# Kernel optimization log

Hardware: AMD Instinct MI355X
Metric: run time of the kernel (lower is better)

## Reference

```python
import jax, jax.numpy as jnp
import numpy as np

D_MODEL = 768
N_HEADS = 8
Q_RANK = 64
KV_RANK = 64
ROPE_DIM = 64
NOPE_DIM = D_MODEL // N_HEADS - ROPE_DIM  # 32
V_DIM = D_MODEL // N_HEADS               # 96
Q_HEAD_DIM = NOPE_DIM + ROPE_DIM         # 96
EPS = 1e-6
ROPE_BASE = 10000.0


def rms_norm(x, w, eps=EPS):
    v = jnp.mean(jnp.square(x.astype(jnp.float32)), axis=-1, keepdims=True)
    return (x.astype(jnp.float32) * jax.lax.rsqrt(v + eps)).astype(x.dtype) * w


def rope_cos_sin(seq_len, dim):
    inv_freq = 1.0 / (ROPE_BASE ** (jnp.arange(0, dim, 2, dtype=jnp.float32) / dim))
    freqs = jnp.outer(jnp.arange(seq_len, dtype=jnp.float32), inv_freq)
    emb = jnp.concatenate([freqs, freqs], axis=-1)  # [s, dim]
    return jnp.cos(emb), jnp.sin(emb)


def apply_rope(x, cos, sin, pos_ids):
    # x: [b,h,s,d]; DeepSeek-V2 de-interleaves pairs before rotate_half
    b, h, s, d = x.shape
    x = x.reshape(b, h, s, d // 2, 2).transpose(0, 1, 2, 4, 3).reshape(b, h, s, d)
    c = cos[pos_ids][:, None]  # [b,1,s,d]
    sn = sin[pos_ids][:, None]
    x1, x2 = jnp.split(x, 2, axis=-1)
    rot = jnp.concatenate([-x2, x1], axis=-1)
    return x * c + rot * sn


def setup_inputs() -> dict:
    key = jax.random.key(0)
    ks = jax.random.split(key, 8)
    s = 0.02
    return {
        "src": jax.random.normal(ks[0], (4, 2048, D_MODEL), jnp.float32),
        "wq_a": jax.random.normal(ks[1], (Q_RANK, D_MODEL), jnp.float32) * s,
        "q_a_ln_w": jnp.ones((Q_RANK,), jnp.float32),
        "wq_b": jax.random.normal(ks[2], (N_HEADS * Q_HEAD_DIM, Q_RANK), jnp.float32) * s,
        "wkv_a": jax.random.normal(ks[3], (KV_RANK + ROPE_DIM, D_MODEL), jnp.float32) * s,
        "kv_a_ln_w": jnp.ones((KV_RANK,), jnp.float32),
        "wkv_b": jax.random.normal(ks[4], (N_HEADS * (NOPE_DIM + V_DIM), KV_RANK), jnp.float32) * s,
        "wo": jax.random.normal(ks[5], (D_MODEL, N_HEADS * V_DIM), jnp.float32) * s,
        "norm_w": jnp.ones((D_MODEL,), jnp.float32),
    }


def reference(src, wq_a, q_a_ln_w, wq_b, wkv_a, kv_a_ln_w, wkv_b, wo, norm_w):
    b, s, _ = src.shape
    pos = jnp.broadcast_to(jnp.arange(s)[None], (b, s))
    cos, sin = rope_cos_sin(s, ROPE_DIM)

    # ---- compress_kv (torch.no_grad in original) ----
    ckv = src @ wkv_a.T                                  # [b,s,rank+rope]
    c_lat, k_pe = ckv[..., :KV_RANK], ckv[..., KV_RANK:]
    c_lat = rms_norm(c_lat, kv_a_ln_w)
    k_pe = apply_rope(k_pe[:, None], cos, sin, pos)[:, 0]  # [b,s,rope]
    c_lat = jax.lax.stop_gradient(c_lat)
    k_pe = jax.lax.stop_gradient(k_pe)

    # ---- query path ----
    q = rms_norm(src @ wq_a.T, q_a_ln_w) @ wq_b.T        # [b,s,h*96]
    q = q.reshape(b, s, N_HEADS, Q_HEAD_DIM).transpose(0, 2, 1, 3)
    q_nope, q_pe = q[..., :NOPE_DIM], q[..., NOPE_DIM:]
    q_pe = apply_rope(q_pe, cos, sin, pos)

    # ---- absorb kv_b_proj ----
    w = wkv_b.reshape(N_HEADS, NOPE_DIM + V_DIM, KV_RANK)
    q_absorb, out_absorb = w[:, :NOPE_DIM], w[:, NOPE_DIM:]   # [h,32,r], [h,96,r]
    q_lat = jnp.einsum('bhsd,hdr->bhsr', q_nope, q_absorb)    # [b,h,s,r]

    scale = Q_HEAD_DIM ** -0.5
    scores = (jnp.einsum('bhsr,btr->bhst', q_lat, c_lat)
              + jnp.einsum('bhsd,btd->bhst', q_pe, k_pe)) * scale
    attn = jax.nn.softmax(scores.astype(jnp.float32), axis=-1).astype(src.dtype)

    ctx = jnp.einsum('bhst,btr->bhsr', attn, c_lat)           # [b,h,s,r]
    ctx = jnp.einsum('bhsr,hvr->bhsv', ctx, out_absorb)       # [b,h,s,96]
    attn_out = ctx.transpose(0, 2, 1, 3).reshape(b, s, N_HEADS * V_DIM) @ wo.T

    # residual (dropout in eval = identity) + RMSNorm
    return rms_norm(src + attn_out, norm_w)
```

## Files before the change

### kernel.cpp

```cpp
#include <hip/hip_runtime.h>


#define DEV static __device__ __forceinline__
typedef unsigned short ushort_t;
typedef __attribute__((ext_vector_type(8))) short bf8_t;
typedef __attribute__((ext_vector_type(4))) float f4_t;

DEV float bf2f(unsigned int u) {
    union { float f; unsigned int i; } x; x.i = u << 16; return x.f;
}
DEV ushort_t f2bf(float f) {
    union { float f; unsigned int u; } x; x.f = f;
    unsigned int u = x.u;
    return (ushort_t)((u + 0x7fffu + ((u >> 16) & 1u)) >> 16);
}
DEV float ldin(const void* p, size_t i, int isbf) {
    return isbf ? bf2f(((const ushort_t*)p)[i]) : ((const float*)p)[i];
}
DEV float fexp2(float x) {
#if __has_builtin(__builtin_amdgcn_exp2f)
    return __builtin_amdgcn_exp2f(x);
#else
    return exp2f(x);
#endif
}
DEV int get_isbf(const void* nw) {
    return ((((const unsigned int*)nw)[0] & 0xffffu) != 0u) ? 1 : 0;
}

constexpr int   TOK   = 4 * 2048;
constexpr float EPSF  = 1e-6f;
constexpr float QSCALE = (float)(0.10206207261596575 * 1.4426950408889634);
constexpr float L2_10000_OVER_32 = 0.4152410118609203f;

constexpr size_t OFF_WOT   = 0;
constexpr size_t OFF_WKVAT = 589824;
constexpr size_t OFF_WQAT  = 688128;
constexpr size_t OFF_WQBT  = 737280;
constexpr size_t OFF_QAF   = 786432;
constexpr size_t OFF_OAT   = 802816;
constexpr size_t OFF_QLN   = 851968;
constexpr size_t OFF_KVLN  = 852032;
constexpr size_t OFF_NW    = 852096;
constexpr size_t OFF_FLAG  = 852864;
constexpr size_t OFF_CTXF  = 852880;
constexpr size_t OFF_SRCBF = 3998608;
constexpr size_t OFF_KBF   = 7144336;
constexpr size_t OFF_VTB   = 7668624;
constexpr size_t OFF_QBF   = 7930768;
constexpr size_t OFF_ROPE  = 12125072;

constexpr int PB0 = 2304;
constexpr int PB1 = PB0 + 384;
constexpr int PB2 = PB1 + 192;
constexpr int PB3 = PB2 + 192;
constexpr int PB4 = PB3 + 64;
constexpr int PB5 = PB4 + 192;
constexpr int PB6 = PB5 + 4;
constexpr int PB7 = PB6 + 256;

__global__ __launch_bounds__(256) void prep_k(
    const void* __restrict__ wq_a, const void* __restrict__ q_ln,
    const void* __restrict__ wq_b, const void* __restrict__ wkv_a,
    const void* __restrict__ kv_ln, const void* __restrict__ wkv_b,
    const void* __restrict__ wo, const void* __restrict__ nw,
    float* __restrict__ ws)
{
    const int isbf = get_isbf(nw);
    const int bid = blockIdx.x;
    const int tid = threadIdx.x;
    if (bid < PB0) {
        int i = bid * 256 + tid;
        ushort_t* wob = (ushort_t*)(ws + OFF_WOT);
        wob[i] = isbf ? ((const ushort_t*)wo)[i] : f2bf(((const float*)wo)[i]);
    } else if (bid < PB1) {
        int i = (bid - PB0) * 256 + tid;
        ushort_t* d = (ushort_t*)(ws + OFF_WKVAT);
        d[i] = isbf ? ((const ushort_t*)wkv_a)[i] : f2bf(((const float*)wkv_a)[i]);
    } else if (bid < PB2) {
        int i = (bid - PB1) * 256 + tid;
        ushort_t* d = (ushort_t*)(ws + OFF_WQAT);
        d[i] = isbf ? ((const ushort_t*)wq_a)[i] : f2bf(((const float*)wq_a)[i]);
    } else if (bid < PB3) {
        int i = (bid - PB2) * 256 + tid;
        ushort_t* d = (ushort_t*)(ws + OFF_WQBT);
        d[i] = isbf ? ((const ushort_t*)wq_b)[i] : f2bf(((const float*)wq_b)[i]);
    } else if (bid < PB4) {
        int i = (bid - PB3) * 256 + tid;
        int h = i >> 11, rem = i & 2047, r = rem >> 5, d = rem & 31;
        ushort_t* dst = (ushort_t*)(ws + OFF_QAF);
        dst[i] = f2bf(ldin(wkv_b, (size_t)(h * 128 + d) * 64 + r, isbf) * QSCALE);
    } else if (bid < PB5) {
        int i = (bid - PB4) * 256 + tid;
        int h = i / 6144, rem = i - h * 6144;
        int r = rem / 96, v = rem - r * 96;
        ws[OFF_OAT + i] = ldin(wkv_b, (size_t)h * 8192 + 2048 + v * 64 + r, isbf);
    } else if (bid < PB6) {
        int i = (bid - PB5) * 256 + tid;
        if (i < 64)             ws[OFF_QLN + i]       = ldin(q_ln, i, isbf);
        else if (i < 128)       ws[OFF_KVLN + i - 64] = ldin(kv_ln, i - 64, isbf);
        else if (i < 128 + 768) ws[OFF_NW + i - 128]  = ldin(nw, i - 128, isbf);
    } else {
        int i = (bid - PB6) * 256 + tid;
        int pos = i >> 5, p = i & 31;
        float inv = exp2f(-(float)p * L2_10000_OVER_32);
        float ang = (float)pos * inv;
        float2* tab = (float2*)(ws + OFF_ROPE);
        tab[i] = make_float2(cosf(ang), sinf(ang));
    }
}

__global__ __launch_bounds__(512) void k1_ckv(
    const void* __restrict__ src, const void* __restrict__ nw,
    const float* __restrict__ ws,
    ushort_t* __restrict__ Kbf, ushort_t* __restrict__ VTbf,
    ushort_t* __restrict__ srcbf)
{
    const ushort_t* wkvab = (const ushort_t*)(ws + OFF_WKVAT);
    const float* kvln  = ws + OFF_KVLN;
    const float2* tab  = (const float2*)(ws + OFF_ROPE);
    const int isbf = get_isbf(nw);
    __shared__ __align__(16) ushort_t sA[32 * 776];
    __shared__ float ckv[32][132];
    int j = threadIdx.x;
    int t0 = blockIdx.x * 32;
    int w = j >> 6, lane = j & 63;
    int tl = lane & 15, qd = lane >> 4;

    {
        for (int e = j; e < 32 * 96; e += 512) {
            int row = e / 96, c8 = e - row * 96;
            size_t off = (size_t)(t0 + row) * 768 + c8 * 8;
            if (isbf) {
                uint4 v = *(const uint4*)((const ushort_t*)src + off);
                *(uint4*)(sA + row * 776 + c8 * 8) = v;
            } else {
                const float4* p = (const float4*)((const float*)src + off);
                float4 f0 = p[0], f1 = p[1];
                ushort_t tmp[8] = {f2bf(f0.x), f2bf(f0.y), f2bf(f0.z), f2bf(f0.w),
                                   f2bf(f1.x), f2bf(f1.y), f2bf(f1.z), f2bf(f1.w)};
                uint4 v = *(const uint4*)tmp;
                *(uint4*)(sA + row * 776 + c8 * 8) = v;
                *(uint4*)(srcbf + off) = v;
            }
        }
    }
    __syncthreads();
    {
        f4_t acc[2];
        acc[0] = (f4_t){0.f, 0.f, 0.f, 0.f};
        acc[1] = (f4_t){0.f, 0.f, 0.f, 0.f};
        const ushort_t* bp = wkvab + (size_t)(w * 16 + tl) * 768 + qd * 8;
#pragma unroll 4
        for (int ks = 0; ks < 24; ++ks) {
            bf8_t b  = *(const bf8_t*)(bp + ks * 32);
            bf8_t a0 = *(const bf8_t*)(sA + tl * 776 + ks * 32 + qd * 8);
            bf8_t a1 = *(const bf8_t*)(sA + (16 + tl) * 776 + ks * 32 + qd * 8);
            acc[0] = __builtin_amdgcn_mfma_f32_16x16x32_bf16(a0, b, acc[0], 0, 0, 0);
            acc[1] = __builtin_amdgcn_mfma_f32_16x16x32_bf16(a1, b, acc[1], 0, 0, 0);
        }
#pragma unroll
        for (int mt = 0; mt < 2; ++mt)
#pragma unroll
            for (int r = 0; r < 4; ++r)
                ckv[mt * 16 + qd * 4 + r][w * 16 + tl] = acc[mt][r];
    }
    __syncthreads();

    if (j < 256) {
        int tt = j >> 3, l = j & 7;
        float ss = 0.f;
#pragma unroll
        for (int i = 0; i < 8; ++i) { float v = ckv[tt][l * 8 + i]; ss += v * v; }
        ss += __shfl_xor(ss, 1); ss += __shfl_xor(ss, 2); ss += __shfl_xor(ss, 4);
        float rs = rsqrtf(ss * (1.f / 64.f) + EPSF);
        size_t base = (size_t)(t0 + tt) * 128;
        ushort_t kb[8];
        float clw[8];
#pragma unroll
        for (int i = 0; i < 8; ++i) {
            int o2 = l * 8 + i;
            float cl = ckv[tt][o2] * rs;
            if (isbf) cl = bf2f(f2bf(cl));
            clw[i] = cl * kvln[o2];
            kb[i] = f2bf(clw[i]);
        }
        uint4 pack;
        pack.x = kb[0] | ((unsigned)kb[1] << 16); pack.y = kb[2] | ((unsigned)kb[3] << 16);
        pack.z = kb[4] | ((unsigned)kb[5] << 16); pack.w = kb[6] | ((unsigned)kb[7] << 16);
        *(uint4*)&Kbf[base + l * 8] = pack;
        int pos = (t0 + tt) & 2047;
        ushort_t r0[4], r1[4];
#pragma unroll
        for (int i = 0; i < 4; ++i) {
            int p = l * 4 + i;
            float2 cssn = tab[pos * 32 + p];
            float e = ckv[tt][64 + 2 * p], od = ckv[tt][64 + 2 * p + 1];
            r0[i] = f2bf(e * cssn.x - od * cssn.y);
            r1[i] = f2bf(od * cssn.x + e * cssn.y);
        }
        uint2 p0, p1;
        p0.x = r0[0] | ((unsigned)r0[1] << 16); p0.y = r0[2] | ((unsigned)r0[3] << 16);
        p1.x = r1[0] | ((unsigned)r1[1] << 16); p1.y = r1[2] | ((unsigned)r1[3] << 16);
        *(uint2*)&Kbf[base + 64 + l * 4] = p0;
        *(uint2*)&Kbf[base + 96 + l * 4] = p1;
#pragma unroll
        for (int i = 0; i < 8; ++i) ckv[tt][l * 8 + i] = clw[i];
    }
    __syncthreads();
    if (j < 256) {
        int t = j & 31, rb = (j >> 5) * 8;
        int bb = t0 >> 11, col = (t0 & 2047) + t;
#pragma unroll
        for (int i = 0; i < 8; ++i) {
            int r = rb + i;
            VTbf[((size_t)(bb * 64 + r)) * 2048 + col] = f2bf(ckv[t][r]);
        }
    }
}

__global__ __launch_bounds__(128) void k2a_qn(
    const void* __restrict__ src, const void* __restrict__ nw,
    const float* __restrict__ ws, ushort_t* __restrict__ qn_all)
{
    const int isbf = get_isbf(nw);
    const ushort_t* srcb = isbf ? (const ushort_t*)src : (const ushort_t*)(ws + OFF_SRCBF);
    const ushort_t* wqab = (const ushort_t*)(ws + OFF_WQAT);
    const float*    qln  = ws + OFF_QLN;
    __shared__ __align__(16) ushort_t LDS[2 * 1152];
    int j = threadIdx.x;
    int w = j >> 6, lane = j & 63;
    int tl = lane & 15, qd = lane >> 4;
    ushort_t* tmpn = LDS + w * 1152;
    int tokw = blockIdx.x * 16;

    f4_t C1[4];
#pragma unroll
    for (int nt = 0; nt < 4; ++nt) C1[nt] = (f4_t){0.f, 0.f, 0.f, 0.f};
    {
        const ushort_t* ap = srcb + (size_t)(tokw + tl) * 768 + qd * 8;
#pragma unroll 4
        for (int ks = 0; ks < 24; ++ks) {
            bf8_t a = *(const bf8_t*)(ap + ks * 32);
#pragma unroll
            for (int nt = 0; nt < 4; ++nt) {
                bf8_t bfr = *(const bf8_t*)(wqab + (size_t)(nt * 16 + tl) * 768 + ks * 32 + qd * 8);
                C1[nt] = __builtin_amdgcn_mfma_f32_16x16x32_bf16(a, bfr, C1[nt], 0, 0, 0);
            }
        }
    }
    float rsv[4];
#pragma unroll
    for (int r = 0; r < 4; ++r) {
        float s = C1[0][r] * C1[0][r] + C1[1][r] * C1[1][r]
                + C1[2][r] * C1[2][r] + C1[3][r] * C1[3][r];
        s += __shfl_xor(s, 1); s += __shfl_xor(s, 2);
        s += __shfl_xor(s, 4); s += __shfl_xor(s, 8);
        rsv[r] = rsqrtf(s * (1.f / 64.f) + EPSF);
    }
    float qlnv[4];
#pragma unroll
    for (int nt = 0; nt < 4; ++nt) qlnv[nt] = qln[nt * 16 + tl];
#pragma unroll
    for (int nt = 0; nt < 4; ++nt)
#pragma unroll
        for (int r = 0; r < 4; ++r) {
            float v = C1[nt][r] * rsv[r];
            if (isbf) v = bf2f(f2bf(v));
            tmpn[(qd * 4 + r) * 72 + nt * 16 + tl] = f2bf(v * qlnv[nt]);
        }
    if (w == 0) {
#pragma unroll
        for (int i = 0; i < 2; ++i) {
            int e = i * 64 + lane;
            int row = e >> 3, ch = e & 7;
            uint4 v = *(const uint4*)(tmpn + row * 72 + ch * 8);
            *(uint4*)(qn_all + (size_t)(tokw + row) * 64 + ch * 8) = v;
        }
    }
}

__global__ __launch_bounds__(512) void k2b_q(
    const float* __restrict__ ws, const ushort_t* __restrict__ qn_all,
    ushort_t* __restrict__ Qbf)
{
    const ushort_t* wqbb = (const ushort_t*)(ws + OFF_WQBT);
    const ushort_t* qabs = (const ushort_t*)(ws + OFF_QAF);
    const float2*   tab  = (const float2*)(ws + OFF_ROPE);

    __shared__ __align__(16) ushort_t sB[384 * 72];
    __shared__ __align__(16) ushort_t sA[32 * 72];
    __shared__ __align__(16) ushort_t PW[8 * 2816];
    int j = threadIdx.x;
    int bx = blockIdx.x;
    int t0 = (bx >> 1) * 32;
    int colh = (bx & 1) * 384;
    int w = j >> 6, lane = j & 63;
    int tl = lane & 15, qd = lane >> 4;
    int mt = w & 1, hh = w >> 1;
    int h = (bx & 1) * 4 + hh;
    ushort_t* qnb = PW + w * 2816;
    ushort_t* qf  = qnb + 640;
    int tokw = t0 + mt * 16;

    {
        for (int e = j; e < 384 * 8; e += 512) {
            int rr = e >> 3, ch = e & 7;
            uint4 v = *(const uint4*)(wqbb + (size_t)(colh + rr) * 64 + ch * 8);
            *(uint4*)(sB + rr * 72 + ch * 8) = v;
        }
    }
    if (j < 256) {
        int rr = j >> 3, ch = j & 7;
        uint4 v = *(const uint4*)(qn_all + (size_t)(t0 + rr) * 64 + ch * 8);
        *(uint4*)(sA + rr * 72 + ch * 8) = v;
    }
    __syncthreads();

    bf8_t A2[2];
#pragma unroll
    for (int ks = 0; ks < 2; ++ks)
        A2[ks] = *(const bf8_t*)(sA + (mt * 16 + tl) * 72 + ks * 32 + qd * 8);

    float csv[4][4], snv[4][4];
#pragma unroll
    for (int nt2 = 0; nt2 < 4; ++nt2) {
        int p = (nt2 * 16 + tl) >> 1;
#pragma unroll
        for (int r = 0; r < 4; ++r) {
            int pos = (tokw + qd * 4 + r) & 2047;
            float2 t = tab[pos * 32 + p];
            csv[nt2][r] = t.x * QSCALE;
            snv[nt2][r] = t.y * QSCALE;
        }
    }
    const bool evn = !(tl & 1);
    int bb = tokw >> 11, pos0 = tokw & 2047;

    f4_t C2[6];
#pragma unroll
    for (int nt = 0; nt < 6; ++nt) C2[nt] = (f4_t){0.f, 0.f, 0.f, 0.f};
#pragma unroll
    for (int nt = 0; nt < 6; ++nt)
#pragma unroll
        for (int ks = 0; ks < 2; ++ks) {
            bf8_t bfr = *(const bf8_t*)(sB + (hh * 96 + nt * 16 + tl) * 72 + ks * 32 + qd * 8);
            C2[nt] = __builtin_amdgcn_mfma_f32_16x16x32_bf16(A2[ks], bfr, C2[nt], 0, 0, 0);
        }
#pragma unroll
    for (int nt = 0; nt < 2; ++nt)
#pragma unroll
        for (int r = 0; r < 4; ++r)
            qnb[(qd * 4 + r) * 40 + nt * 16 + tl] = f2bf(C2[nt][r]);
    bf8_t an = *(const bf8_t*)(qnb + tl * 40 + qd * 8);
    f4_t C3[4];
#pragma unroll
    for (int nt = 0; nt < 4; ++nt) C3[nt] = (f4_t){0.f, 0.f, 0.f, 0.f};
#pragma unroll
    for (int nt = 0; nt < 4; ++nt) {
        bf8_t bfr = *(const bf8_t*)(qabs + (size_t)h * 2048 + (nt * 16 + tl) * 32 + qd * 8);
        C3[nt] = __builtin_amdgcn_mfma_f32_16x16x32_bf16(an, bfr, C3[nt], 0, 0, 0);
    }
#pragma unroll
    for (int nt = 0; nt < 4; ++nt)
#pragma unroll
        for (int r = 0; r < 4; ++r)
            qf[(qd * 4 + r) * 136 + nt * 16 + tl] = f2bf(C3[nt][r]);
#pragma unroll
    for (int nt2 = 0; nt2 < 4; ++nt2) {
        int p = (nt2 * 16 + tl) >> 1;
        int outc = evn ? (64 + p) : (96 + p);
#pragma unroll
        for (int r = 0; r < 4; ++r) {
            float val = C2[nt2 + 2][r];
            float part = __shfl_xor(val, 1);
            float res = evn ? (val * csv[nt2][r] - part * snv[nt2][r])
                            : (val * csv[nt2][r] + part * snv[nt2][r]);
            qf[(qd * 4 + r) * 136 + outc] = f2bf(res);
        }
    }
    size_t qb = ((size_t)(bb * 8 + h) * 2048 + pos0) * 128;
#pragma unroll
    for (int i = 0; i < 4; ++i) {
        int idx = i * 64 + lane;
        int row = idx >> 4, c = idx & 15;
        uint4 v = *(const uint4*)(qf + row * 136 + c * 8);
        *(uint4*)(Qbf + qb + (size_t)row * 128 + c * 8) = v;
    }
}

__global__ __launch_bounds__(256, 2) void k3_attn(
    const ushort_t* __restrict__ Qbf, const ushort_t* __restrict__ Kbf,
    const ushort_t* __restrict__ VTbf, const float* __restrict__ oaT,
    ushort_t* __restrict__ ctxb)
{
    __shared__ __align__(16) ushort_t LDS[22528];
    ushort_t* Kt = LDS;
    ushort_t* Vt = LDS + 8704;
    ushort_t* Pw = LDS + 13312;
    int j = threadIdx.x;
    int b = blockIdx.z, h = blockIdx.y, q0g = blockIdx.x * 128;
    int w = j >> 6, lane = j & 63;
    int tl = lane & 15, qd = lane >> 4;
    ushort_t* Pme = Pw + w * 2304;
    int qw = q0g + w * 32;

    bf8_t qfA[4], qfB[4];
    {
        const ushort_t* qp = Qbf + ((size_t)((b * 8 + h) * 2048) + qw + tl) * 128 + qd * 8;
#pragma unroll
        for (int ks = 0; ks < 4; ++ks) {
            qfA[ks] = *(const bf8_t*)(qp + ks * 32);
            qfB[ks] = *(const bf8_t*)(qp + 16 * 128 + ks * 32);
        }
    }
    f4_t OaccA[4], OaccB[4];
#pragma unroll
    for (int nt = 0; nt < 4; ++nt) {
        OaccA[nt] = (f4_t){0.f, 0.f, 0.f, 0.f};
        OaccB[nt] = (f4_t){0.f, 0.f, 0.f, 0.f};
    }
    float lA = 0.f, lB = 0.f;

    const size_t kbase = (size_t)b * 2048 * 128;
    const size_t vbase = (size_t)b * 64 * 2048;

    for (int it = 0; it < 32; ++it) {
        __syncthreads();
        {
            int r = j >> 2, c0 = (j & 3) * 32;
            const uint4* gp = (const uint4*)(Kbf + kbase + (size_t)(it * 64 + r) * 128 + c0);
            uint4 a0 = gp[0], a1 = gp[1], a2 = gp[2], a3 = gp[3];
            uint4* dp = (uint4*)(Kt + r * 136 + c0);
            dp[0] = a0; dp[1] = a1; dp[2] = a2; dp[3] = a3;
        }
        {
            int d = j >> 2, c0 = (j & 3) * 16;
            const uint4* gp = (const uint4*)(VTbf + vbase + (size_t)d * 2048 + it * 64 + c0);
            uint4 a0 = gp[0], a1 = gp[1];
            uint4* dp = (uint4*)(Vt + d * 72 + c0);
            dp[0] = a0; dp[1] = a1;
        }
        __syncthreads();
        f4_t SA[4], SB[4];
        __builtin_amdgcn_s_setprio(1);
#pragma unroll
        for (int nt = 0; nt < 4; ++nt) {
            f4_t cA = (f4_t){0.f, 0.f, 0.f, 0.f};
            f4_t cB = (f4_t){0.f, 0.f, 0.f, 0.f};
#pragma unroll
            for (int ks = 0; ks < 4; ++ks) {
                bf8_t kf = *(const bf8_t*)(Kt + (nt * 16 + tl) * 136 + ks * 32 + qd * 8);
                cA = __builtin_amdgcn_mfma_f32_16x16x32_bf16(kf, qfA[ks], cA, 0, 0, 0);
                cB = __builtin_amdgcn_mfma_f32_16x16x32_bf16(kf, qfB[ks], cB, 0, 0, 0);
            }
            SA[nt] = cA; SB[nt] = cB;
        }
        __builtin_amdgcn_s_setprio(0);
        float rsA = 0.f, rsB = 0.f;
#pragma unroll
        for (int nt = 0; nt < 4; ++nt)
#pragma unroll
            for (int r = 0; r < 4; ++r) {
                float pA = fexp2(SA[nt][r]); SA[nt][r] = pA; rsA += pA;
                float pB = fexp2(SB[nt][r]); SB[nt][r] = pB; rsB += pB;
            }
        rsA += __shfl_xor(rsA, 16); rsA += __shfl_xor(rsA, 32);
        rsB += __shfl_xor(rsB, 16); rsB += __shfl_xor(rsB, 32);
        lA += rsA; lB += rsB;
#pragma unroll
        for (int nt = 0; nt < 4; ++nt) {
            uint2 pkA, pkB;
            pkA.x = f2bf(SA[nt][0]) | ((unsigned)f2bf(SA[nt][1]) << 16);
            pkA.y = f2bf(SA[nt][2]) | ((unsigned)f2bf(SA[nt][3]) << 16);
            pkB.x = f2bf(SB[nt][0]) | ((unsigned)f2bf(SB[nt][1]) << 16);
            pkB.y = f2bf(SB[nt][2]) | ((unsigned)f2bf(SB[nt][3]) << 16);
            *(uint2*)(Pme + tl * 72 + nt * 16 + qd * 4) = pkA;
            *(uint2*)(Pme + (16 + tl) * 72 + nt * 16 + qd * 4) = pkB;
        }
        bf8_t pfA[2], pfB[2];
#pragma unroll
        for (int ks = 0; ks < 2; ++ks) {
            pfA[ks] = *(const bf8_t*)(Pme + tl * 72 + ks * 32 + qd * 8);
            pfB[ks] = *(const bf8_t*)(Pme + (16 + tl) * 72 + ks * 32 + qd * 8);
        }
        __builtin_amdgcn_s_setprio(1);
#pragma unroll
        for (int nt = 0; nt < 4; ++nt)
#pragma unroll
            for (int ks = 0; ks < 2; ++ks) {
                bf8_t vf = *(const bf8_t*)(Vt + (nt * 16 + tl) * 72 + ks * 32 + qd * 8);
                OaccA[nt] = __builtin_amdgcn_mfma_f32_16x16x32_bf16(pfA[ks], vf, OaccA[nt], 0, 0, 0);
                OaccB[nt] = __builtin_amdgcn_mfma_f32_16x16x32_bf16(pfB[ks], vf, OaccB[nt], 0, 0, 0);
            }
        __builtin_amdgcn_s_setprio(0);
    }
    {
        float linvA[4], linvB[4];
#pragma unroll
        for (int r = 0; r < 4; ++r) {
            float lqA = __shfl(lA, (lane & 48) + qd * 4 + r);
            float lqB = __shfl(lB, (lane & 48) + qd * 4 + r);
            linvA[r] = 1.f / lqA; linvB[r] = 1.f / lqB;
        }
#pragma unroll
        for (int nt = 0; nt < 4; ++nt)
#pragma unroll
            for (int r = 0; r < 4; ++r) {
                Pme[(qd * 4 + r) * 72 + nt * 16 + tl] = f2bf(OaccA[nt][r] * linvA[r]);
                Pme[(16 + qd * 4 + r) * 72 + nt * 16 + tl] = f2bf(OaccB[nt][r] * linvB[r]);
            }
    }
    __syncthreads();
    ushort_t* OA = LDS;
    for (int e = j; e < 96 * 64; e += 256) {
        int v = e >> 6, r = e & 63;
        OA[v * 72 + r] = f2bf(oaT[h * 6144 + r * 96 + v]);
    }
    __syncthreads();
    {
        bf8_t ofA[2], ofB[2];
#pragma unroll
        for (int ks = 0; ks < 2; ++ks) {
            ofA[ks] = *(const bf8_t*)(Pme + tl * 72 + ks * 32 + qd * 8);
            ofB[ks] = *(const bf8_t*)(Pme + (16 + tl) * 72 + ks * 32 + qd * 8);
        }
        __builtin_amdgcn_s_setprio(1);
#pragma unroll
        for (int nt = 0; nt < 6; ++nt) {
            f4_t cA = (f4_t){0.f, 0.f, 0.f, 0.f};
            f4_t cB = (f4_t){0.f, 0.f, 0.f, 0.f};
#pragma unroll
            for (int ks = 0; ks < 2; ++ks) {
                bf8_t af = *(const bf8_t*)(OA + (nt * 16 + tl) * 72 + ks * 32 + qd * 8);
                cA = __builtin_amdgcn_mfma_f32_16x16x32_bf16(ofA[ks], af, cA, 0, 0, 0);
                cB = __builtin_amdgcn_mfma_f32_16x16x32_bf16(ofB[ks], af, cB, 0, 0, 0);
            }
#pragma unroll
            for (int r = 0; r < 4; ++r) {
                size_t tokA = (size_t)(b * 2048 + qw + qd * 4 + r);
                size_t tokB = tokA + 16;
                ctxb[tokA * 768 + h * 96 + nt * 16 + tl] = f2bf(cA[r]);
                ctxb[tokB * 768 + h * 96 + nt * 16 + tl] = f2bf(cB[r]);
            }
        }
        __builtin_amdgcn_s_setprio(0);
    }
}

__global__ __launch_bounds__(512, 2) void k5a_gemm(
    const void* __restrict__ src, const void* __restrict__ nw,
    const float* __restrict__ ws,
    const ushort_t* __restrict__ ctxb, ushort_t* __restrict__ ybf)
{
    const ushort_t* woB = (const ushort_t*)(ws + OFF_WOT);
    const int isbf = get_isbf(nw);
    __shared__ __align__(16) ushort_t sB[384 * 72];
    __shared__ __align__(16) ushort_t sA[32 * 72];
    int j = threadIdx.x;
    int bx = blockIdx.x;
    int t0 = (bx >> 1) * 32;
    int colh = (bx & 1) * 384;
    int w = j >> 6, lane = j & 63;
    int tl = lane & 15, qd = lane >> 4;
    int mt = w & 1;
    int n0l = (w >> 1) * 96;

    f4_t acc[6];
#pragma unroll
    for (int nt = 0; nt < 6; ++nt) acc[nt] = (f4_t){0.f, 0.f, 0.f, 0.f};

    for (int kb = 0; kb < 12; ++kb) {
        __syncthreads();
        {
            for (int e = j; e < 384 * 8; e += 512) {
                int rr = e >> 3, ch = e & 7;
                uint4 v = *(const uint4*)(woB + (size_t)(colh + rr) * 768 + kb * 64 + ch * 8);
                *(uint4*)(sB + rr * 72 + ch * 8) = v;
            }
        }
        if (j < 256) {
            int rr = j >> 3, ch = j & 7;
            uint4 v = *(const uint4*)(ctxb + (size_t)(t0 + rr) * 768 + kb * 64 + ch * 8);
            *(uint4*)(sA + rr * 72 + ch * 8) = v;
        }
        __syncthreads();
        __builtin_amdgcn_s_setprio(1);
#pragma unroll
        for (int ks = 0; ks < 2; ++ks) {
            bf8_t a = *(const bf8_t*)(sA + (mt * 16 + tl) * 72 + ks * 32 + qd * 8);
#pragma unroll
            for (int nt = 0; nt < 6; ++nt) {
                bf8_t bfr = *(const bf8_t*)(sB + (n0l + nt * 16 + tl) * 72 + ks * 32 + qd * 8);
                acc[nt] = __builtin_amdgcn_mfma_f32_16x16x32_bf16(a, bfr, acc[nt], 0, 0, 0);
            }
        }
        __builtin_amdgcn_s_setprio(0);
    }
#pragma unroll
    for (int nt = 0; nt < 6; ++nt)
#pragma unroll
        for (int r = 0; r < 4; ++r) {
            int row = t0 + mt * 16 + qd * 4 + r;
            int col = colh + n0l + nt * 16 + tl;
            float yv = acc[nt][r] + ldin(src, (size_t)row * 768 + col, isbf);
            ybf[(size_t)row * 768 + col] = f2bf(yv);
        }
}

__global__ __launch_bounds__(256) void k5b_norm(
    const void* __restrict__ nw_in, const float* __restrict__ ws,
    const ushort_t* __restrict__ ybf, void* __restrict__ out)
{
    const float* nw = ws + OFF_NW;
    const int isbf = get_isbf(nw_in);
    int j = threadIdx.x;
    int tt = j >> 4, s = j & 15;
    size_t row = (size_t)blockIdx.x * 16 + tt;
    const ushort_t* yp = ybf + row * 768 + s * 48;

    float val[48];
    float ss = 0.f;
#pragma unroll
    for (int c8 = 0; c8 < 6; ++c8) {
        union { uint4 u; ushort_t h[8]; } uu;
        uu.u = ((const uint4*)yp)[c8];
#pragma unroll
        for (int c = 0; c < 8; ++c) {
            float v = bf2f(uu.h[c]);
            val[c8 * 8 + c] = v;
            ss += v * v;
        }
    }
    ss += __shfl_xor(ss, 1); ss += __shfl_xor(ss, 2);
    ss += __shfl_xor(ss, 4); ss += __shfl_xor(ss, 8);
    float rs = rsqrtf(ss * (1.f / 768.f) + EPSF);
    const float* nwp = nw + s * 48;
    size_t base = row * 768 + s * 48;
    if (isbf) {
        ushort_t* op = (ushort_t*)out + base;
#pragma unroll
        for (int c8 = 0; c8 < 6; ++c8) {
            union { uint4 u; ushort_t h[8]; } uu;
#pragma unroll
            for (int c = 0; c < 8; ++c) {
                float hv = bf2f(f2bf(val[c8 * 8 + c] * rs));
                uu.h[c] = f2bf(hv * nwp[c8 * 8 + c]);
            }
            ((uint4*)op)[c8] = uu.u;
        }
    } else {
        float* op = (float*)out + base;
#pragma unroll
        for (int c4 = 0; c4 < 12; ++c4) {
            float4 f;
            f.x = val[c4 * 4 + 0] * rs * nwp[c4 * 4 + 0];
            f.y = val[c4 * 4 + 1] * rs * nwp[c4 * 4 + 1];
            f.z = val[c4 * 4 + 2] * rs * nwp[c4 * 4 + 2];
            f.w = val[c4 * 4 + 3] * rs * nwp[c4 * 4 + 3];
            ((float4*)op)[c4] = f;
        }
    }
}

extern "C" void kernel_launch(void* const* d_in, const int* in_sizes, int n_in,
                              void* d_out, int out_size, void* d_ws, size_t ws_size,
                              hipStream_t stream)
{
    const void* src   = d_in[0];
    const void* wq_a  = d_in[1];
    const void* q_ln  = d_in[2];
    const void* wq_b  = d_in[3];
    const void* wkv_a = d_in[4];
    const void* kv_ln = d_in[5];
    const void* wkv_b = d_in[6];
    const void* wo    = d_in[7];
    const void* nw    = d_in[8];
    float* ws = (float*)d_ws;
    ushort_t* Kbf   = (ushort_t*)(ws + OFF_KBF);
    ushort_t* VTbf  = (ushort_t*)(ws + OFF_VTB);
    ushort_t* Qbf   = (ushort_t*)(ws + OFF_QBF);
    ushort_t* ctxb  = (ushort_t*)(ws + OFF_CTXF);
    ushort_t* srcbf = (ushort_t*)(ws + OFF_SRCBF);
    ushort_t* ybf   = Qbf;
    ushort_t* qn    = ctxb;

    prep_k<<<dim3(PB7), dim3(256), 0, stream>>>(wq_a, q_ln, wq_b, wkv_a, kv_ln, wkv_b, wo, nw, ws);
    k1_ckv<<<dim3(TOK / 32), dim3(512), 0, stream>>>(src, nw, ws, Kbf, VTbf, srcbf);
    k2a_qn<<<dim3(TOK / 16), dim3(128), 0, stream>>>(src, nw, ws, qn);
    k2b_q<<<dim3(TOK / 32 * 2), dim3(512), 0, stream>>>(ws, qn, Qbf);
    k3_attn<<<dim3(16, 8, 4), dim3(256), 0, stream>>>(Qbf, Kbf, VTbf, ws + OFF_OAT, ctxb);
    k5a_gemm<<<dim3(TOK / 32 * 2), dim3(512), 0, stream>>>(src, nw, ws, ctxb, ybf);
    k5b_norm<<<dim3(TOK / 16), dim3(256), 0, stream>>>(nw, ws, ybf, d_out);
}
```

Before: 260.5 us.

## Load K/V MFMA fragments directly from global memory, dropping LDS staging and barriers

The attention kernel no longer stages K and V tiles through shared memory with two barriers per iteration. Each wave now loads its MFMA operand fragments straight from global memory (cached via L1/L2). The out-absorb weight tile is moved to the kernel start so the LDS region can be reused, which shrinks LDS and removes the syncs after the loop. In exchange, each of the four waves reloads the same K/V data, so L2 traffic goes up, and global load latency is now exposed right before the MFMAs with no prefetch.

```diff
diff --git a/kernel.cpp b/kernel.cpp
--- a/kernel.cpp
+++ b/kernel.cpp
@@ -394,10 +394,9 @@
     const ushort_t* __restrict__ VTbf, const float* __restrict__ oaT,
     ushort_t* __restrict__ ctxb)
 {
-    __shared__ __align__(16) ushort_t LDS[22528];
-    ushort_t* Kt = LDS;
-    ushort_t* Vt = LDS + 8704;
-    ushort_t* Pw = LDS + 13312;
+    __shared__ __align__(16) ushort_t LDS[16128];
+    ushort_t* Pw = LDS;
+    ushort_t* OA = LDS + 9216;
     int j = threadIdx.x;
     int b = blockIdx.z, h = blockIdx.y, q0g = blockIdx.x * 128;
     int w = j >> 6, lane = j & 63;
@@ -405,6 +404,11 @@
     ushort_t* Pme = Pw + w * 2304;
     int qw = q0g + w * 32;
 
+    for (int e = j; e < 96 * 64; e += 256) {
+        int v = e >> 6, r = e & 63;
+        OA[v * 72 + r] = f2bf(oaT[h * 6144 + r * 96 + v]);
+    }
+
     bf8_t qfA[4], qfB[4];
     {
         const ushort_t* qp = Qbf + ((size_t)((b * 8 + h) * 2048) + qw + tl) * 128 + qd * 8;
@@ -422,41 +426,31 @@
     }
     float lA = 0.f, lB = 0.f;
 
-    const size_t kbase = (size_t)b * 2048 * 128;
-    const size_t vbase = (size_t)b * 64 * 2048;
+    const ushort_t* kfp = Kbf + (size_t)b * 2048 * 128 + (size_t)tl * 128 + qd * 8;
+    const ushort_t* vfp = VTbf + (size_t)b * 64 * 2048 + (size_t)tl * 2048 + qd * 8;
+
+    __syncthreads();
 
     for (int it = 0; it < 32; ++it) {
-        __syncthreads();
-        {
-            int r = j >> 2, c0 = (j & 3) * 32;
-            const uint4* gp = (const uint4*)(Kbf + kbase + (size_t)(it * 64 + r) * 128 + c0);
-            uint4 a0 = gp[0], a1 = gp[1], a2 = gp[2], a3 = gp[3];
-            uint4* dp = (uint4*)(Kt + r * 136 + c0);
-            dp[0] = a0; dp[1] = a1; dp[2] = a2; dp[3] = a3;
-        }
-        {
-            int d = j >> 2, c0 = (j & 3) * 16;
-            const uint4* gp = (const uint4*)(VTbf + vbase + (size_t)d * 2048 + it * 64 + c0);
-            uint4 a0 = gp[0], a1 = gp[1];
-            uint4* dp = (uint4*)(Vt + d * 72 + c0);
-            dp[0] = a0; dp[1] = a1;
-        }
-        __syncthreads();
         f4_t SA[4], SB[4];
-        __builtin_amdgcn_s_setprio(1);
+        const ushort_t* kt = kfp + (size_t)(it * 64) * 128;
 #pragma unroll
         for (int nt = 0; nt < 4; ++nt) {
+            bf8_t kfr[4];
+#pragma unroll
+            for (int ks = 0; ks < 4; ++ks)
+                kfr[ks] = *(const bf8_t*)(kt + (size_t)(nt * 16) * 128 + ks * 32);
             f4_t cA = (f4_t){0.f, 0.f, 0.f, 0.f};
             f4_t cB = (f4_t){0.f, 0.f, 0.f, 0.f};
+            __builtin_amdgcn_s_setprio(1);
 #pragma unroll
             for (int ks = 0; ks < 4; ++ks) {
-                bf8_t kf = *(const bf8_t*)(Kt + (nt * 16 + tl) * 136 + ks * 32 + qd * 8);
-                cA = __builtin_amdgcn_mfma_f32_16x16x32_bf16(kf, qfA[ks], cA, 0, 0, 0);
-                cB = __builtin_amdgcn_mfma_f32_16x16x32_bf16(kf, qfB[ks], cB, 0, 0, 0);
-            }
+                cA = __builtin_amdgcn_mfma_f32_16x16x32_bf16(kfr[ks], qfA[ks], cA, 0, 0, 0);
+                cB = __builtin_amdgcn_mfma_f32_16x16x32_bf16(kfr[ks], qfB[ks], cB, 0, 0, 0);
+            }
+            __builtin_amdgcn_s_setprio(0);
             SA[nt] = cA; SB[nt] = cB;
         }
-        __builtin_amdgcn_s_setprio(0);
         float rsA = 0.f, rsB = 0.f;
 #pragma unroll
         for (int nt = 0; nt < 4; ++nt)
@@ -484,16 +478,21 @@
             pfA[ks] = *(const bf8_t*)(Pme + tl * 72 + ks * 32 + qd * 8);
             pfB[ks] = *(const bf8_t*)(Pme + (16 + tl) * 72 + ks * 32 + qd * 8);
         }
-        __builtin_amdgcn_s_setprio(1);
-#pragma unroll
-        for (int nt = 0; nt < 4; ++nt)
+        const ushort_t* vt = vfp + it * 64;
+#pragma unroll
+        for (int nt = 0; nt < 4; ++nt) {
+            bf8_t vfr[2];
+#pragma unroll
+            for (int ks = 0; ks < 2; ++ks)
+                vfr[ks] = *(const bf8_t*)(vt + (size_t)(nt * 16) * 2048 + ks * 32);
+            __builtin_amdgcn_s_setprio(1);
 #pragma unroll
             for (int ks = 0; ks < 2; ++ks) {
-                bf8_t vf = *(const bf8_t*)(Vt + (nt * 16 + tl) * 72 + ks * 32 + qd * 8);
-                OaccA[nt] = __builtin_amdgcn_mfma_f32_16x16x32_bf16(pfA[ks], vf, OaccA[nt], 0, 0, 0);
-                OaccB[nt] = __builtin_amdgcn_mfma_f32_16x16x32_bf16(pfB[ks], vf, OaccB[nt], 0, 0, 0);
-            }
-        __builtin_amdgcn_s_setprio(0);
+                OaccA[nt] = __builtin_amdgcn_mfma_f32_16x16x32_bf16(pfA[ks], vfr[ks], OaccA[nt], 0, 0, 0);
+                OaccB[nt] = __builtin_amdgcn_mfma_f32_16x16x32_bf16(pfB[ks], vfr[ks], OaccB[nt], 0, 0, 0);
+            }
+            __builtin_amdgcn_s_setprio(0);
+        }
     }
     {
         float linvA[4], linvB[4];
@@ -511,13 +510,6 @@
                 Pme[(16 + qd * 4 + r) * 72 + nt * 16 + tl] = f2bf(OaccB[nt][r] * linvB[r]);
             }
     }
-    __syncthreads();
-    ushort_t* OA = LDS;
-    for (int e = j; e < 96 * 64; e += 256) {
-        int v = e >> 6, r = e & 63;
-        OA[v * 72 + r] = f2bf(oaT[h * 6144 + r * 96 + v]);
-    }
-    __syncthreads();
     {
         bf8_t ofA[2], ofB[2];
 #pragma unroll
```

Result: slower. 368.1 us (+41.3%).
